# Kernel optimization log

Measured on AMD Instinct MI355X. Metric: run time of the kernel, lower is better.

## Reference

```python
import jax, jax.numpy as jnp
import numpy as np

RR = 0.5  # residual_rate for this layer


def setup_inputs() -> dict:
    key = jax.random.key(0)
    k0, k1, k2, k3, k4 = jax.random.split(key, 5)
    B, IN_PN, OUT_PN, M, CIN, COUT = 64, 20000, 5000, 9, 32, 64
    AVG_NB = float(M)
    in_pc = jax.random.normal(k0, (B, IN_PN, CIN), jnp.float32)
    # neighbor ids in [0, IN_PN]; value IN_PN is the zero-padding index
    neighbor_id = jax.random.randint(k1, (OUT_PN, M), 0, IN_PN + 1)
    weights = jax.random.normal(k2, (OUT_PN, M, COUT, CIN), jnp.float32) / AVG_NB
    bias = jnp.zeros((OUT_PN, COUT), jnp.float32)  # perpoint_bias == 1
    p_neighbors = jax.random.normal(k3, (OUT_PN, M), jnp.float32) / AVG_NB
    weight_res = jax.random.normal(k4, (COUT, CIN), jnp.float32) / COUT
    return dict(in_pc=in_pc, neighbor_id=neighbor_id, weights=weights,
                bias=bias, p_neighbors=p_neighbors, weight_res=weight_res)


def reference(in_pc, neighbor_id, weights, bias, p_neighbors, weight_res):
    B, in_pn, cin = in_pc.shape
    out_pn, M = neighbor_id.shape
    # pad with a zero point so index == in_pn gathers zeros (pc_mask trick)
    in_pc_pad = jnp.concatenate(
        [in_pc, jnp.zeros((B, 1, cin), in_pc.dtype)], axis=1)
    in_neighbors = in_pc_pad[:, neighbor_id]          # [B, out_pn, M, cin]
    # vertex-wise weighted conv: per-output-point, per-neighbor weight matrix
    out_conv = jnp.einsum('bpmc,pmoc->bpo', in_neighbors, weights) + bias
    out_conv = jax.nn.elu(out_conv)                   # self.relu = nn.ELU()
    # residual (pooling) path: learned normalized neighbor weighting
    neighbor_mask = (neighbor_id != in_pn).astype(in_pc.dtype)  # [out_pn, M]
    p = jnp.abs(p_neighbors) * neighbor_mask
    p = p / (p.sum(axis=1, keepdims=True) + 1e-8)
    out_res = jnp.einsum('pm,bpmc->bpc', p, in_neighbors)       # [B, out_pn, cin]
    out_res = jnp.einsum('bpc,oc->bpo', out_res, weight_res)    # channel lift
    return out_conv * np.float32(np.sqrt(1.0 - RR)) + out_res * np.float32(np.sqrt(RR))
```

## Files before the change

kernel.cpp:

```cpp
#include <hip/hip_runtime.h>
#include <cmath>

#define IN_PN   20000
#define OUT_PN  5000
#define MM      9
#define CIN     32
#define COUT    64

typedef short        bf16x8 __attribute__((ext_vector_type(8)));
typedef float        f32x16 __attribute__((ext_vector_type(16)));
typedef unsigned int u32x4  __attribute__((ext_vector_type(4)));

__device__ __forceinline__ unsigned pack_bf16_hi(float x0, float x1) {
    return __builtin_amdgcn_perm(__float_as_uint(x1), __float_as_uint(x0), 0x07060302u);
}
__device__ __forceinline__ float bf16_trunc(float x) {
    return __uint_as_float(__float_as_uint(x) & 0xFFFF0000u);
}
__device__ __forceinline__ bf16x8 frag(u32x4 u) {
    return __builtin_bit_cast(bf16x8, u);
}
__device__ __forceinline__ void split8(const float* x, u32x4& hi, u32x4& lo) {
#pragma unroll
    for (int i = 0; i < 4; ++i) {
        float x0 = x[2 * i], x1 = x[2 * i + 1];
        hi[i] = pack_bf16_hi(x0, x1);
        lo[i] = pack_bf16_hi(x0 - bf16_trunc(x0), x1 - bf16_trunc(x1));
    }
}

__global__ __launch_bounds__(256, 4) void pconv_kernel(
    const float* __restrict__ in_pc,
    const int*   __restrict__ neighbor_id,
    const float* __restrict__ weights,
    const float* __restrict__ bias,
    const float* __restrict__ p_neighbors,
    const float* __restrict__ weight_res,
    float*       __restrict__ out)
{
    const int p    = blockIdx.x;
    const int t    = threadIdx.x;
    const int lane = t & 63;
    const int wv   = t >> 6;
    const int wr   = wv >> 1;
    const int wc   = wv & 1;
    const int l32  = lane & 31;
    const int lh   = lane >> 5;

    int   nid[MM];
    float pn[MM];
    float psum = 0.f;
#pragma unroll
    for (int m = 0; m < MM; ++m) {
        nid[m] = neighbor_id[p * MM + m];
        float pv = fabsf(p_neighbors[p * MM + m]);
        pv = (nid[m] != IN_PN) ? pv : 0.f;
        pn[m] = pv;
        psum += pv;
    }
    const float pinv = 1.f / (psum + 1e-8f);
#pragma unroll
    for (int m = 0; m < MM; ++m) pn[m] *= pinv;

    const int brow = wr * 32 + l32;
    const int ocol = wc * 32 + l32;

    const float* Abase = in_pc   + (size_t)brow * (IN_PN * CIN) + lh * 8;
    const float* Bbase = weights + (size_t)p * (MM * COUT * CIN) + (size_t)ocol * CIN + lh * 8;

    f32x16 accC, accR;
#pragma unroll
    for (int j = 0; j < 16; ++j) { accC[j] = 0.f; accR[j] = 0.f; }
    float rv[2][8];
#pragma unroll
    for (int i = 0; i < 2; ++i)
#pragma unroll
        for (int e = 0; e < 8; ++e) rv[i][e] = 0.f;

#pragma unroll
    for (int m = 0; m < MM; ++m) {
        const int   n  = nid[m];
        const float pm = pn[m];
        float xa[16], wb[16];
        if (n != IN_PN) {
            const float* a = Abase + (size_t)n * CIN;
            float4 t0 = *(const float4*)(a);
            float4 t1 = *(const float4*)(a + 4);
            float4 t2 = *(const float4*)(a + 16);
            float4 t3 = *(const float4*)(a + 20);
            xa[0]=t0.x;  xa[1]=t0.y;  xa[2]=t0.z;  xa[3]=t0.w;
            xa[4]=t1.x;  xa[5]=t1.y;  xa[6]=t1.z;  xa[7]=t1.w;
            xa[8]=t2.x;  xa[9]=t2.y;  xa[10]=t2.z; xa[11]=t2.w;
            xa[12]=t3.x; xa[13]=t3.y; xa[14]=t3.z; xa[15]=t3.w;
        } else {
#pragma unroll
            for (int e = 0; e < 16; ++e) xa[e] = 0.f;
        }
        {
            const float* bsp = Bbase + m * (COUT * CIN);
            float4 s0 = *(const float4*)(bsp);
            float4 s1 = *(const float4*)(bsp + 4);
            float4 s2 = *(const float4*)(bsp + 16);
            float4 s3 = *(const float4*)(bsp + 20);
            wb[0]=s0.x;  wb[1]=s0.y;  wb[2]=s0.z;  wb[3]=s0.w;
            wb[4]=s1.x;  wb[5]=s1.y;  wb[6]=s1.z;  wb[7]=s1.w;
            wb[8]=s2.x;  wb[9]=s2.y;  wb[10]=s2.z; wb[11]=s2.w;
            wb[12]=s3.x; wb[13]=s3.y; wb[14]=s3.z; wb[15]=s3.w;
        }

#pragma unroll
        for (int par = 0; par < 2; ++par) {
#pragma unroll
            for (int e = 0; e < 8; ++e) rv[par][e] += pm * xa[par * 8 + e];

            u32x4 ah, al, bh, bl;
            split8(&xa[par * 8], ah, al);
            split8(&wb[par * 8], bh, bl);
            accC = __builtin_amdgcn_mfma_f32_32x32x16_bf16(frag(ah), frag(bh), accC, 0, 0, 0);
            accC = __builtin_amdgcn_mfma_f32_32x32x16_bf16(frag(ah), frag(bl), accC, 0, 0, 0);
            accC = __builtin_amdgcn_mfma_f32_32x32x16_bf16(frag(al), frag(bh), accC, 0, 0, 0);
        }
    }

    {
        const float* wrb = weight_res + (size_t)ocol * CIN + lh * 8;
#pragma unroll
        for (int kk = 0; kk < 2; ++kk) {
            float wb2[8];
            float4 s0 = *(const float4*)(wrb + kk * 16);
            float4 s1 = *(const float4*)(wrb + kk * 16 + 4);
            wb2[0]=s0.x; wb2[1]=s0.y; wb2[2]=s0.z; wb2[3]=s0.w;
            wb2[4]=s1.x; wb2[5]=s1.y; wb2[6]=s1.z; wb2[7]=s1.w;
            u32x4 ah, al, bh, bl;
            split8(&rv[kk][0], ah, al);
            split8(&wb2[0], bh, bl);
            accR = __builtin_amdgcn_mfma_f32_32x32x16_bf16(frag(ah), frag(bh), accR, 0, 0, 0);
            accR = __builtin_amdgcn_mfma_f32_32x32x16_bf16(frag(ah), frag(bl), accR, 0, 0, 0);
            accR = __builtin_amdgcn_mfma_f32_32x32x16_bf16(frag(al), frag(bh), accR, 0, 0, 0);
        }
    }

    const float bv = bias[p * COUT + ocol];
    float* obase = out + (size_t)p * COUT + ocol;
#pragma unroll
    for (int j = 0; j < 16; ++j) {
        const int br = wr * 32 + (j & 3) + 8 * (j >> 2) + 4 * lh;
        float cv = accC[j] + bv;
        cv = (cv > 0.f) ? cv : expm1f(cv);
        obase[(size_t)br * (OUT_PN * COUT)] = 0.70710678118654752f * (cv + accR[j]);
    }
}

extern "C" void kernel_launch(void* const* d_in, const int* in_sizes, int n_in,
                              void* d_out, int out_size, void* d_ws, size_t ws_size,
                              hipStream_t stream) {
    const float* in_pc       = (const float*)d_in[0];
    const int*   neighbor_id = (const int*)d_in[1];
    const float* weights     = (const float*)d_in[2];
    const float* bias        = (const float*)d_in[3];
    const float* p_neighbors = (const float*)d_in[4];
    const float* weight_res  = (const float*)d_in[5];
    float*       out         = (float*)d_out;

    pconv_kernel<<<OUT_PN, 256, 0, stream>>>(in_pc, neighbor_id, weights, bias,
                                             p_neighbors, weight_res, out);
}
```

Measured before the change: 761.7 us.

## Double-buffer gather loads and stage output through LDS for vectorized stores

```diff
diff --git a/kernel.cpp b/kernel.cpp
--- a/kernel.cpp
+++ b/kernel.cpp
@@ -6,6 +6,7 @@
 #define MM      9
 #define CIN     32
 #define COUT    64
+#define OUT_STRIDE 68
 
 typedef short        bf16x8 __attribute__((ext_vector_type(8)));
 typedef float        f32x16 __attribute__((ext_vector_type(16)));
@@ -17,16 +18,20 @@
 __device__ __forceinline__ float bf16_trunc(float x) {
     return __uint_as_float(__float_as_uint(x) & 0xFFFF0000u);
 }
-__device__ __forceinline__ bf16x8 frag(u32x4 u) {
-    return __builtin_bit_cast(bf16x8, u);
-}
-__device__ __forceinline__ void split8(const float* x, u32x4& hi, u32x4& lo) {
-#pragma unroll
-    for (int i = 0; i < 4; ++i) {
-        float x0 = x[2 * i], x1 = x[2 * i + 1];
-        hi[i] = pack_bf16_hi(x0, x1);
-        lo[i] = pack_bf16_hi(x0 - bf16_trunc(x0), x1 - bf16_trunc(x1));
-    }
+__device__ __forceinline__ bf16x8 frag(u32x4 u) { return __builtin_bit_cast(bf16x8, u); }
+
+__device__ __forceinline__ void split_pair(float4 u, float4 v, u32x4& hi, u32x4& lo) {
+    hi[0] = pack_bf16_hi(u.x, u.y);
+    hi[1] = pack_bf16_hi(u.z, u.w);
+    hi[2] = pack_bf16_hi(v.x, v.y);
+    hi[3] = pack_bf16_hi(v.z, v.w);
+    lo[0] = pack_bf16_hi(u.x - bf16_trunc(u.x), u.y - bf16_trunc(u.y));
+    lo[1] = pack_bf16_hi(u.z - bf16_trunc(u.z), u.w - bf16_trunc(u.w));
+    lo[2] = pack_bf16_hi(v.x - bf16_trunc(v.x), v.y - bf16_trunc(v.y));
+    lo[3] = pack_bf16_hi(v.z - bf16_trunc(v.z), v.w - bf16_trunc(v.w));
+}
+__device__ __forceinline__ float uniform_f(float x) {
+    return __uint_as_float(__builtin_amdgcn_readfirstlane(__float_as_uint(x)));
 }
 
 __global__ __launch_bounds__(256, 4) void pconv_kernel(
@@ -38,6 +43,7 @@
     const float* __restrict__ weight_res,
     float*       __restrict__ out)
 {
+    __shared__ float smem[64 * OUT_STRIDE];
     const int p    = blockIdx.x;
     const int t    = threadIdx.x;
     const int lane = t & 63;
@@ -52,7 +58,7 @@
     float psum = 0.f;
 #pragma unroll
     for (int m = 0; m < MM; ++m) {
-        nid[m] = neighbor_id[p * MM + m];
+        nid[m] = __builtin_amdgcn_readfirstlane(neighbor_id[p * MM + m]);
         float pv = fabsf(p_neighbors[p * MM + m]);
         pv = (nid[m] != IN_PN) ? pv : 0.f;
         pn[m] = pv;
@@ -60,94 +66,121 @@
     }
     const float pinv = 1.f / (psum + 1e-8f);
 #pragma unroll
-    for (int m = 0; m < MM; ++m) pn[m] *= pinv;
+    for (int m = 0; m < MM; ++m) pn[m] = uniform_f(pn[m] * pinv);
 
     const int brow = wr * 32 + l32;
     const int ocol = wc * 32 + l32;
 
-    const float* Abase = in_pc   + (size_t)brow * (IN_PN * CIN) + lh * 8;
-    const float* Bbase = weights + (size_t)p * (MM * COUT * CIN) + (size_t)ocol * CIN + lh * 8;
-
-    f32x16 accC, accR;
-#pragma unroll
-    for (int j = 0; j < 16; ++j) { accC[j] = 0.f; accR[j] = 0.f; }
-    float rv[2][8];
-#pragma unroll
-    for (int i = 0; i < 2; ++i)
-#pragma unroll
-        for (int e = 0; e < 8; ++e) rv[i][e] = 0.f;
+    const float* Abase = in_pc      + (size_t)brow * (IN_PN * CIN) + lh * 8;
+    const float* Bbase = weights    + (size_t)p * (MM * COUT * CIN) + (size_t)ocol * CIN + lh * 8;
+    const float* wrb   = weight_res + (size_t)ocol * CIN + lh * 8;
+
+    float4 Abuf[2][4], Bbuf[2][4];
+    const float4 zero4 = make_float4(0.f, 0.f, 0.f, 0.f);
+
+#define LOADA(buf_, m_) do {                                           \
+        const int n_ = nid[m_];                                        \
+        if (n_ != IN_PN) {                                             \
+            const float* a_ = Abase + (size_t)n_ * CIN;                \
+            Abuf[buf_][0] = *(const float4*)(a_);                      \
+            Abuf[buf_][1] = *(const float4*)(a_ + 4);                  \
+            Abuf[buf_][2] = *(const float4*)(a_ + 16);                 \
+            Abuf[buf_][3] = *(const float4*)(a_ + 20);                 \
+        } else {                                                       \
+            Abuf[buf_][0] = zero4; Abuf[buf_][1] = zero4;              \
+            Abuf[buf_][2] = zero4; Abuf[buf_][3] = zero4;              \
+        }                                                              \
+    } while (0)
+#define LOADB(buf_, m_) do {                                           \
+        const float* b_ = Bbase + (m_) * (COUT * CIN);                 \
+        Bbuf[buf_][0] = *(const float4*)(b_);                          \
+        Bbuf[buf_][1] = *(const float4*)(b_ + 4);                      \
+        Bbuf[buf_][2] = *(const float4*)(b_ + 16);                     \
+        Bbuf[buf_][3] = *(const float4*)(b_ + 20);                     \
+    } while (0)
+
+    f32x16 accC;
+#pragma unroll
+    for (int j = 0; j < 16; ++j) accC[j] = 0.f;
+    float4 rva[4];
+#pragma unroll
+    for (int i = 0; i < 4; ++i) rva[i] = zero4;
+
+    float bv = 0.f;
+    LOADA(0, 0);
+    LOADB(0, 0);
 
 #pragma unroll
     for (int m = 0; m < MM; ++m) {
-        const int   n  = nid[m];
+        const int cur = m & 1;
+        const int nxt = cur ^ 1;
+        if (m + 1 < MM) {
+            LOADA(nxt, m + 1);
+            LOADB(nxt, m + 1);
+        } else {
+            Bbuf[nxt][0] = *(const float4*)(wrb);
+            Bbuf[nxt][1] = *(const float4*)(wrb + 4);
+            Bbuf[nxt][2] = *(const float4*)(wrb + 16);
+            Bbuf[nxt][3] = *(const float4*)(wrb + 20);
+            bv = bias[p * COUT + ocol];
+        }
+
         const float pm = pn[m];
-        float xa[16], wb[16];
-        if (n != IN_PN) {
-            const float* a = Abase + (size_t)n * CIN;
-            float4 t0 = *(const float4*)(a);
-            float4 t1 = *(const float4*)(a + 4);
-            float4 t2 = *(const float4*)(a + 16);
-            float4 t3 = *(const float4*)(a + 20);
-            xa[0]=t0.x;  xa[1]=t0.y;  xa[2]=t0.z;  xa[3]=t0.w;
-            xa[4]=t1.x;  xa[5]=t1.y;  xa[6]=t1.z;  xa[7]=t1.w;
-            xa[8]=t2.x;  xa[9]=t2.y;  xa[10]=t2.z; xa[11]=t2.w;
-            xa[12]=t3.x; xa[13]=t3.y; xa[14]=t3.z; xa[15]=t3.w;
-        } else {
-#pragma unroll
-            for (int e = 0; e < 16; ++e) xa[e] = 0.f;
+#pragma unroll
+        for (int i = 0; i < 4; ++i) {
+            rva[i].x += pm * Abuf[cur][i].x;
+            rva[i].y += pm * Abuf[cur][i].y;
+            rva[i].z += pm * Abuf[cur][i].z;
+            rva[i].w += pm * Abuf[cur][i].w;
         }
-        {
-            const float* bsp = Bbase + m * (COUT * CIN);
-            float4 s0 = *(const float4*)(bsp);
-            float4 s1 = *(const float4*)(bsp + 4);
-            float4 s2 = *(const float4*)(bsp + 16);
-            float4 s3 = *(const float4*)(bsp + 20);
-            wb[0]=s0.x;  wb[1]=s0.y;  wb[2]=s0.z;  wb[3]=s0.w;
-            wb[4]=s1.x;  wb[5]=s1.y;  wb[6]=s1.z;  wb[7]=s1.w;
-            wb[8]=s2.x;  wb[9]=s2.y;  wb[10]=s2.z; wb[11]=s2.w;
-            wb[12]=s3.x; wb[13]=s3.y; wb[14]=s3.z; wb[15]=s3.w;
-        }
-
-#pragma unroll
-        for (int par = 0; par < 2; ++par) {
-#pragma unroll
-            for (int e = 0; e < 8; ++e) rv[par][e] += pm * xa[par * 8 + e];
-
-            u32x4 ah, al, bh, bl;
-            split8(&xa[par * 8], ah, al);
-            split8(&wb[par * 8], bh, bl);
-            accC = __builtin_amdgcn_mfma_f32_32x32x16_bf16(frag(ah), frag(bh), accC, 0, 0, 0);
-            accC = __builtin_amdgcn_mfma_f32_32x32x16_bf16(frag(ah), frag(bl), accC, 0, 0, 0);
-            accC = __builtin_amdgcn_mfma_f32_32x32x16_bf16(frag(al), frag(bh), accC, 0, 0, 0);
-        }
-    }
-
+
+        u32x4 ah, al, bh, bl;
+        split_pair(Abuf[cur][0], Abuf[cur][1], ah, al);
+        split_pair(Bbuf[cur][0], Bbuf[cur][1], bh, bl);
+        accC = __builtin_amdgcn_mfma_f32_32x32x16_bf16(frag(ah), frag(bh), accC, 0, 0, 0);
+        accC = __builtin_amdgcn_mfma_f32_32x32x16_bf16(frag(ah), frag(bl), accC, 0, 0, 0);
+        accC = __builtin_amdgcn_mfma_f32_32x32x16_bf16(frag(al), frag(bh), accC, 0, 0, 0);
+        split_pair(Abuf[cur][2], Abuf[cur][3], ah, al);
+        split_pair(Bbuf[cur][2], Bbuf[cur][3], bh, bl);
+        accC = __builtin_amdgcn_mfma_f32_32x32x16_bf16(frag(ah), frag(bh), accC, 0, 0, 0);
+        accC = __builtin_amdgcn_mfma_f32_32x32x16_bf16(frag(ah), frag(bl), accC, 0, 0, 0);
+        accC = __builtin_amdgcn_mfma_f32_32x32x16_bf16(frag(al), frag(bh), accC, 0, 0, 0);
+    }
+#undef LOADA
+#undef LOADB
+
+    f32x16 accR;
+#pragma unroll
+    for (int j = 0; j < 16; ++j) accR[j] = 0.f;
     {
-        const float* wrb = weight_res + (size_t)ocol * CIN + lh * 8;
-#pragma unroll
-        for (int kk = 0; kk < 2; ++kk) {
-            float wb2[8];
-            float4 s0 = *(const float4*)(wrb + kk * 16);
-            float4 s1 = *(const float4*)(wrb + kk * 16 + 4);
-            wb2[0]=s0.x; wb2[1]=s0.y; wb2[2]=s0.z; wb2[3]=s0.w;
-            wb2[4]=s1.x; wb2[5]=s1.y; wb2[6]=s1.z; wb2[7]=s1.w;
-            u32x4 ah, al, bh, bl;
-            split8(&rv[kk][0], ah, al);
-            split8(&wb2[0], bh, bl);
-            accR = __builtin_amdgcn_mfma_f32_32x32x16_bf16(frag(ah), frag(bh), accR, 0, 0, 0);
-            accR = __builtin_amdgcn_mfma_f32_32x32x16_bf16(frag(ah), frag(bl), accR, 0, 0, 0);
-            accR = __builtin_amdgcn_mfma_f32_32x32x16_bf16(frag(al), frag(bh), accR, 0, 0, 0);
-        }
-    }
-
-    const float bv = bias[p * COUT + ocol];
-    float* obase = out + (size_t)p * COUT + ocol;
+        u32x4 ah, al, bh, bl;
+        split_pair(rva[0], rva[1], ah, al);
+        split_pair(Bbuf[1][0], Bbuf[1][1], bh, bl);
+        accR = __builtin_amdgcn_mfma_f32_32x32x16_bf16(frag(ah), frag(bh), accR, 0, 0, 0);
+        accR = __builtin_amdgcn_mfma_f32_32x32x16_bf16(frag(ah), frag(bl), accR, 0, 0, 0);
+        accR = __builtin_amdgcn_mfma_f32_32x32x16_bf16(frag(al), frag(bh), accR, 0, 0, 0);
+        split_pair(rva[2], rva[3], ah, al);
+        split_pair(Bbuf[1][2], Bbuf[1][3], bh, bl);
+        accR = __builtin_amdgcn_mfma_f32_32x32x16_bf16(frag(ah), frag(bh), accR, 0, 0, 0);
+        accR = __builtin_amdgcn_mfma_f32_32x32x16_bf16(frag(ah), frag(bl), accR, 0, 0, 0);
+        accR = __builtin_amdgcn_mfma_f32_32x32x16_bf16(frag(al), frag(bh), accR, 0, 0, 0);
+    }
+
 #pragma unroll
     for (int j = 0; j < 16; ++j) {
         const int br = wr * 32 + (j & 3) + 8 * (j >> 2) + 4 * lh;
         float cv = accC[j] + bv;
         cv = (cv > 0.f) ? cv : expm1f(cv);
-        obase[(size_t)br * (OUT_PN * COUT)] = 0.70710678118654752f * (cv + accR[j]);
+        smem[br * OUT_STRIDE + ocol] = 0.70710678118654752f * (cv + accR[j]);
+    }
+    __syncthreads();
+
+    const int bb = t >> 2;
+    const int q  = t & 3;
+#pragma unroll
+    for (int s = 0; s < 4; ++s) {
+        float4 v = *(const float4*)&smem[bb * OUT_STRIDE + q * 16 + s * 4];
+        *(float4*)&out[((size_t)bb * OUT_PN + (size_t)p) * COUT + q * 16 + s * 4] = v;
     }
 }
 
```

New measurement: 812.4 us. 1.07x slower.
